# Kernel optimization log

Measured on AMD Instinct MI355X. Metric: run time of the kernel, lower is better.

The kernel has to match this reference:

```python
import jax, jax.numpy as jnp
import numpy as np

NUM_GRAPHS = 256
BN_EPS = 1e-5


def _bn(x, g, b, m, v):
    # eval-mode BatchNorm1d: affine with running stats
    return (x - m) * jax.lax.rsqrt(v + BN_EPS) * g + b


def setup_inputs() -> dict:
    key = jax.random.key(0)
    ks = jax.random.split(key, 16)
    N = 500_000
    x = jax.random.normal(ks[0], (N, 3), dtype=jnp.float32)
    batch = jnp.sort(jax.random.randint(ks[1], (N,), 0, NUM_GRAPHS, dtype=jnp.int32))

    def lin(k, fan_in, fan_out):
        kw, kb = jax.random.split(k)
        s = 1.0 / np.sqrt(fan_in)
        W = jax.random.uniform(kw, (fan_in, fan_out), jnp.float32, -s, s)
        b = jax.random.uniform(kb, (fan_out,), jnp.float32, -s, s)
        return W, b

    def bn_params(k, dim):
        k1, k2, k3, k4 = jax.random.split(k, 4)
        g = 1.0 + 0.05 * jax.random.normal(k1, (dim,), jnp.float32)
        be = 0.05 * jax.random.normal(k2, (dim,), jnp.float32)
        m = 0.05 * jax.random.normal(k3, (dim,), jnp.float32)
        v = 0.5 + jax.random.uniform(k4, (dim,), jnp.float32)
        return g, be, m, v

    W1, b1 = lin(ks[2], 3, 64)
    g1, be1, m1, v1 = bn_params(ks[3], 64)
    W2, b2 = lin(ks[4], 64, 64)          # plain last layer of local MLP
    W3, b3 = lin(ks[5], 64, 128)
    g3, be3, m3, v3 = bn_params(ks[6], 128)
    W4, b4 = lin(ks[7], 128, 1024)       # plain last layer of global MLP

    return {
        "x": x, "batch": batch,
        "W1": W1, "b1": b1, "g1": g1, "be1": be1, "m1": m1, "v1": v1,
        "W2": W2, "b2": b2,
        "W3": W3, "b3": b3, "g3": g3, "be3": be3, "m3": m3, "v3": v3,
        "W4": W4, "b4": b4,
    }


def reference(x, batch, W1, b1, g1, be1, m1, v1, W2, b2,
              W3, b3, g3, be3, m3, v3, W4, b4):
    # local MLP [3, 64, 64]: Linear->BN->ReLU, plain last
    h = jax.nn.relu(_bn(x @ W1 + b1, g1, be1, m1, v1))   # [N, 64]
    h = h @ W2 + b2                                       # [N, 64]
    # global MLP [64, 128, 1024]: Linear->BN->ReLU, plain last
    h = jax.nn.relu(_bn(h @ W3 + b3, g3, be3, m3, v3))    # [N, 128]
    h = h @ W4 + b4                                       # [N, 1024]
    # global_max_pool: ragged scatter-max over per-point graph ids
    out = jax.ops.segment_max(h, batch, num_segments=NUM_GRAPHS)  # [G, 1024]
    return out
```

## Files before the change

kernel.cpp:

```cpp
#include <hip/hip_runtime.h>
#include <hip/hip_bf16.h>
#include <cstdint>

typedef __attribute__((ext_vector_type(8))) short bf16x8;
typedef __attribute__((ext_vector_type(4))) float f32x4;

#define BN_EPS 1e-5f

__device__ __forceinline__ unsigned short f2bf(float f) {
    unsigned int u = __float_as_uint(f);
    unsigned int r = (u + 0x7FFFu + ((u >> 16) & 1u)) >> 16;
    return (unsigned short)r;
}
__device__ __forceinline__ float bf2f(unsigned short h) {
    return __uint_as_float(((unsigned int)h) << 16);
}
__device__ __forceinline__ unsigned int encf(float f) {
    unsigned int u = __float_as_uint(f);
    return (u & 0x80000000u) ? ~u : (u | 0x80000000u);
}

__device__ __forceinline__ long long lbound(const int* __restrict__ b, long long n, int key) {
    long long lo = 0, hi = n;
    while (lo < hi) { long long mid = (lo + hi) >> 1; if (b[mid] < key) lo = mid + 1; else hi = mid; }
    return lo;
}

__global__ void fold_kernel(const float* __restrict__ W1, const float* __restrict__ b1,
                            const float* __restrict__ g1, const float* __restrict__ be1,
                            const float* __restrict__ m1, const float* __restrict__ v1,
                            const float* __restrict__ W2, const float* __restrict__ b2,
                            const float* __restrict__ W3, const float* __restrict__ b3,
                            const float* __restrict__ g3, const float* __restrict__ be3,
                            const float* __restrict__ m3, const float* __restrict__ v3,
                            const float* __restrict__ W4,
                            unsigned short* __restrict__ W4p,
                            unsigned short* __restrict__ W23ph, unsigned short* __restrict__ W23pl,
                            float* __restrict__ W1c, float* __restrict__ b23) {
    int tid = blockIdx.x * blockDim.x + threadIdx.x;
    if (tid < 131072) {
        int j = tid & 7, lane = (tid >> 3) & 63, kf = (tid >> 9) & 3, nt = tid >> 11;
        int col = nt * 16 + (lane & 15);
        int k = kf * 32 + (lane >> 4) * 8 + j;
        W4p[tid] = f2bf(W4[k * 1024 + col]);
    }
    if (tid < 8192) {
        int j = tid & 7, lane = (tid >> 3) & 63, kf = (tid >> 9) & 1, nn = tid >> 10;
        int col = nn * 16 + (lane & 15);
        int k = kf * 32 + (lane >> 4) * 8 + j;
        float s3 = g3[col] / sqrtf(v3[col] + BN_EPS);
        float acc = 0.f;
        for (int o = 0; o < 64; ++o) acc += W2[k * 64 + o] * W3[o * 128 + col];
        float w = acc * s3;
        unsigned short hi = f2bf(w);
        W23ph[tid] = hi;
        W23pl[tid] = f2bf(w - bf2f(hi));
    }
    if (tid < 128) {
        float s3 = g3[tid] / sqrtf(v3[tid] + BN_EPS);
        float acc = b3[tid] - m3[tid];
        for (int o = 0; o < 64; ++o) acc += b2[o] * W3[o * 128 + tid];
        b23[tid] = acc * s3 + be3[tid];
    }
    if (tid < 256) {
        int o = tid >> 2, c = tid & 3;
        float s1 = g1[o] / sqrtf(v1[o] + BN_EPS);
        W1c[tid] = (c < 3) ? W1[c * 64 + o] * s1 : (b1[o] - m1[o]) * s1 + be1[o];
    }
}

__global__ __launch_bounds__(64, 4) void fused_kernel(const float* __restrict__ x,
                                                      const float* __restrict__ W1c,
                                                      const unsigned short* __restrict__ W23ph,
                                                      const unsigned short* __restrict__ W23pl,
                                                      const float* __restrict__ b23,
                                                      const unsigned short* __restrict__ W4p,
                                                      const float* __restrict__ b4,
                                                      const int* __restrict__ batch,
                                                      unsigned int* __restrict__ out,
                                                      float* __restrict__ tilemax,
                                                      int* __restrict__ gtile,
                                                      long long pbase, int ntiles, long long Ntot) {
    __shared__ unsigned short h3[64 * 72];
    int wave = blockIdx.x;
    if (wave >= ntiles) return;
    int lane = threadIdx.x & 63;
    int q = lane >> 4, r16 = lane & 15;
    long long p0 = pbase + (long long)wave * 64;

    float xv[4][3];
    bool valid[4];
#pragma unroll
    for (int mt = 0; mt < 4; ++mt) {
        long long p = p0 + mt * 16 + r16;
        if (p < Ntot) {
            xv[mt][0] = x[p * 3 + 0]; xv[mt][1] = x[p * 3 + 1]; xv[mt][2] = x[p * 3 + 2];
            valid[mt] = true;
        } else {
            xv[mt][0] = xv[mt][1] = xv[mt][2] = 0.f; valid[mt] = false;
        }
    }
    bf16x8 a2[4][2];
#pragma unroll
    for (int kf = 0; kf < 2; ++kf)
#pragma unroll
        for (int j = 0; j < 8; ++j) {
            int f = kf * 32 + q * 8 + j;
            float4 w = *reinterpret_cast<const float4*>(W1c + f * 4);
#pragma unroll
            for (int mt = 0; mt < 4; ++mt) {
                float v = fmaf(xv[mt][0], w.x, fmaf(xv[mt][1], w.y, fmaf(xv[mt][2], w.z, w.w)));
                v = valid[mt] ? fmaxf(v, 0.f) : 0.f;
                a2[mt][kf][j] = (short)f2bf(v);
            }
        }

    bf16x8 a[4][4];
#pragma unroll
    for (int half = 0; half < 2; ++half) {
#pragma unroll
        for (int n = 0; n < 4; ++n) {
            int nn = half * 4 + n;
            f32x4 acc2[4];
#pragma unroll
            for (int mt = 0; mt < 4; ++mt) acc2[mt] = (f32x4){0.f, 0.f, 0.f, 0.f};
#pragma unroll
            for (int kf = 0; kf < 2; ++kf) {
                bf16x8 bh = *reinterpret_cast<const bf16x8*>(W23ph + (size_t)((nn * 2 + kf) * 64 + lane) * 8);
                bf16x8 bl = *reinterpret_cast<const bf16x8*>(W23pl + (size_t)((nn * 2 + kf) * 64 + lane) * 8);
#pragma unroll
                for (int mt = 0; mt < 4; ++mt) {
                    acc2[mt] = __builtin_amdgcn_mfma_f32_16x16x32_bf16(a2[mt][kf], bh, acc2[mt], 0, 0, 0);
                    acc2[mt] = __builtin_amdgcn_mfma_f32_16x16x32_bf16(a2[mt][kf], bl, acc2[mt], 0, 0, 0);
                }
            }
            int col = nn * 16 + r16;
            float bias = b23[col];
#pragma unroll
            for (int mt = 0; mt < 4; ++mt)
#pragma unroll
                for (int r = 0; r < 4; ++r) {
                    int row = mt * 16 + q * 4 + r;
                    float v = fmaxf(acc2[mt][r] + bias, 0.f);
                    h3[row * 72 + n * 16 + r16] = f2bf(v);
                }
        }
        asm volatile("s_waitcnt lgkmcnt(0)" ::: "memory");
#pragma unroll
        for (int mt = 0; mt < 4; ++mt)
#pragma unroll
            for (int kfl = 0; kfl < 2; ++kfl)
                a[mt][half * 2 + kfl] =
                    *reinterpret_cast<const bf16x8*>(h3 + (16 * mt + r16) * 72 + kfl * 32 + q * 8);
        asm volatile("s_waitcnt lgkmcnt(0)" ::: "memory");
    }

    long long plast = p0 + 63; if (plast > Ntot - 1) plast = Ntot - 1;
    int gfirst = batch[(p0 < Ntot) ? p0 : (Ntot - 1)];
    int glast = batch[plast];
    bool fast = (gfirst == glast) && (p0 + 63 < Ntot);
    if (lane == 0) gtile[wave] = fast ? gfirst : -1;

    if (fast) {
        float* tm = tilemax + (size_t)wave * 1024;
        const unsigned short* wp = W4p + (size_t)lane * 8;
        bf16x8 Bp[2][4];
#pragma unroll
        for (int kf = 0; kf < 4; ++kf)
            Bp[0][kf] = *reinterpret_cast<const bf16x8*>(wp + (size_t)kf * 512);

        for (int g8 = 0; g8 < 8; ++g8) {
            float m8[8];
#pragma unroll
            for (int i8 = 0; i8 < 8; ++i8) {
                int nt = g8 * 8 + i8;
                const int cur = i8 & 1, nxt = cur ^ 1;
                {
                    const unsigned short* wq = wp + (size_t)(((nt + 1) & 63) * 4) * 512;
#pragma unroll
                    for (int kf = 0; kf < 4; ++kf)
                        Bp[nxt][kf] = *reinterpret_cast<const bf16x8*>(wq + (size_t)kf * 512);
                }
                f32x4 acc[4];
#pragma unroll
                for (int mt = 0; mt < 4; ++mt) acc[mt] = (f32x4){0.f, 0.f, 0.f, 0.f};
#pragma unroll
                for (int kf = 0; kf < 4; ++kf)
#pragma unroll
                    for (int mt = 0; mt < 4; ++mt)
                        acc[mt] = __builtin_amdgcn_mfma_f32_16x16x32_bf16(a[mt][kf], Bp[cur][kf], acc[mt], 0, 0, 0);
                float m = fmaxf(fmaxf(fmaxf(acc[0][0], acc[0][1]), fmaxf(acc[0][2], acc[0][3])),
                                fmaxf(fmaxf(acc[1][0], acc[1][1]), fmaxf(acc[1][2], acc[1][3])));
                m = fmaxf(m, fmaxf(fmaxf(fmaxf(acc[2][0], acc[2][1]), fmaxf(acc[2][2], acc[2][3])),
                                   fmaxf(fmaxf(acc[3][0], acc[3][1]), fmaxf(acc[3][2], acc[3][3]))));
                m8[i8] = m;
            }
#pragma unroll
            for (int qq = 0; qq < 8; ++qq) {
                float v = m8[qq];
                v = fmaxf(v, __shfl_xor(v, 16));
                v = fmaxf(v, __shfl_xor(v, 32));
                m8[qq] = v;
            }
            if (lane < 16) {
#pragma unroll
                for (int qq = 0; qq < 8; ++qq) tm[(g8 * 8 + qq) * 16 + lane] = m8[qq];
            }
        }
        return;
    }

    int gl = -1;
    unsigned long long smask = 0;
    int grow[16];
    {
        long long pl = p0 + lane;
        gl = (pl < Ntot) ? batch[pl] : -1;
        int gprev = __shfl_up(gl, 1);
        bool is_start = (lane == 0) || (gl != gprev);
        smask = __ballot(is_start);
#pragma unroll
        for (int m = 0; m < 4; ++m)
#pragma unroll
            for (int r = 0; r < 4; ++r) {
                int rw = m * 16 + (lane >> 4) * 4 + r;
                grow[m * 4 + r] = __shfl(gl, rw);
            }
    }

    for (int nt = 0; nt < 64; ++nt) {
        bf16x8 bq[4];
#pragma unroll
        for (int kf = 0; kf < 4; ++kf)
            bq[kf] = *reinterpret_cast<const bf16x8*>(W4p + (size_t)((nt * 4 + kf) * 64 + lane) * 8);
        f32x4 acc[4];
#pragma unroll
        for (int m = 0; m < 4; ++m) acc[m] = (f32x4){0.f, 0.f, 0.f, 0.f};
#pragma unroll
        for (int kf = 0; kf < 4; ++kf)
#pragma unroll
            for (int m = 0; m < 4; ++m)
                acc[m] = __builtin_amdgcn_mfma_f32_16x16x32_bf16(a[m][kf], bq[kf], acc[m], 0, 0, 0);

        int col = nt * 16 + (lane & 15);
        float bias = b4[col];
        unsigned long long tmp = smask;
        while (tmp) {
            int ls = __builtin_ctzll(tmp); tmp &= tmp - 1;
            int gs = __shfl(gl, ls);
            float m = -INFINITY;
#pragma unroll
            for (int mm = 0; mm < 4; ++mm)
#pragma unroll
                for (int r = 0; r < 4; ++r)
                    if (grow[mm * 4 + r] == gs) m = fmaxf(m, acc[mm][r]);
            m = fmaxf(m, __shfl_xor(m, 16));
            m = fmaxf(m, __shfl_xor(m, 32));
            if (gs >= 0 && lane < 16 && m > -INFINITY)
                atomicMax(&out[gs * 1024 + col], encf(m + bias));
        }
    }
}

__global__ __launch_bounds__(256) void reduce_chunk(const float* __restrict__ tilemax,
                                                    const int* __restrict__ gtile,
                                                    const int* __restrict__ batch,
                                                    const float* __restrict__ b4,
                                                    unsigned int* __restrict__ out,
                                                    long long base, long long npts, long long N) {
    int g = blockIdx.x >> 2;
    int col = (blockIdx.x & 3) * 256 + threadIdx.x;
    __shared__ int sh[2];
    if (threadIdx.x == 0) {
        long long lo = lbound(batch, N, g);
        long long hi = lbound(batch, N, g + 1);
        long long e = base + npts;
        if (lo < base) lo = base;
        if (hi > e) hi = e;
        sh[0] = (int)(lo - base);
        sh[1] = (int)(hi - base);
    }
    __syncthreads();
    int lo = sh[0], hi = sh[1];
    if (lo >= hi) return;
    int t0 = lo >> 6, t1 = (hi - 1) >> 6;
    float m = -INFINITY;
    for (int t = t0; t <= t1; ++t)
        if (gtile[t] == g) m = fmaxf(m, tilemax[(size_t)t * 1024 + col]);
    if (m > -INFINITY) atomicMax(&out[g * 1024 + col], encf(m + b4[col]));
}

__global__ void init_out(unsigned int* out, int n) {
    int t = blockIdx.x * 256 + threadIdx.x;
    if (t < n) out[t] = 0x007FFFFFu;
}
__global__ void decode_out(unsigned int* out, int n) {
    int t = blockIdx.x * 256 + threadIdx.x;
    if (t < n) {
        unsigned int e = out[t];
        out[t] = (e & 0x80000000u) ? (e & 0x7FFFFFFFu) : ~e;
    }
}

extern "C" void kernel_launch(void* const* d_in, const int* in_sizes, int n_in,
                              void* d_out, int out_size, void* d_ws, size_t ws_size,
                              hipStream_t stream) {
    const float* x   = (const float*)d_in[0];
    const int* batch = (const int*)d_in[1];
    const float* W1  = (const float*)d_in[2];
    const float* b1  = (const float*)d_in[3];
    const float* g1  = (const float*)d_in[4];
    const float* be1 = (const float*)d_in[5];
    const float* m1  = (const float*)d_in[6];
    const float* v1  = (const float*)d_in[7];
    const float* W2  = (const float*)d_in[8];
    const float* b2  = (const float*)d_in[9];
    const float* W3  = (const float*)d_in[10];
    const float* b3  = (const float*)d_in[11];
    const float* g3  = (const float*)d_in[12];
    const float* be3 = (const float*)d_in[13];
    const float* m3  = (const float*)d_in[14];
    const float* v3  = (const float*)d_in[15];
    const float* W4  = (const float*)d_in[16];
    const float* b4  = (const float*)d_in[17];

    long long N = in_sizes[1];

    char* ws = (char*)d_ws;
    unsigned short* W4p   = (unsigned short*)(ws + 0);
    unsigned short* W23ph = (unsigned short*)(ws + 262144);
    unsigned short* W23pl = (unsigned short*)(ws + 278528);
    float* W1c = (float*)(ws + 294912);
    float* b23 = (float*)(ws + 295936);

    fold_kernel<<<512, 256, 0, stream>>>(W1, b1, g1, be1, m1, v1, W2, b2, W3, b3, g3, be3, m3, v3,
                                         W4, W4p, W23ph, W23pl, W1c, b23);
    init_out<<<(out_size + 255) / 256, 256, 0, stream>>>((unsigned int*)d_out, out_size);

    const size_t ofs = 1 << 20;
    size_t avail = (ws_size > ofs) ? ws_size - ofs : 0;
    long long Tcap = (long long)(avail / 4104);
    Tcap &= ~3LL;
    if (Tcap < 4) Tcap = 4;
    long long ntiles_tot = (N + 63) / 64;
    long long ntcap = (ntiles_tot + 3) & ~3LL;
    if (Tcap > ntcap) Tcap = ntcap;

    float* tilemax = (float*)(ws + ofs);
    int* gtile = (int*)(ws + ofs + (size_t)Tcap * 4096);
    long long chunk = Tcap * 64;

    for (long long base = 0; base < N; base += chunk) {
        long long npts = N - base; if (npts > chunk) npts = chunk;
        int ntiles = (int)((npts + 63) / 64);
        fused_kernel<<<ntiles, 64, 0, stream>>>(x, W1c, W23ph, W23pl, b23, W4p, b4, batch,
                                                (unsigned int*)d_out, tilemax, gtile,
                                                base, ntiles, N);
        reduce_chunk<<<1024, 256, 0, stream>>>(tilemax, gtile, batch, b4, (unsigned int*)d_out,
                                               base, npts, N);
    }
    decode_out<<<(out_size + 255) / 256, 256, 0, stream>>>((unsigned int*)d_out, out_size);
}
```

Baseline: 207.6 us.

## Share W4 tiles across four waves via double-buffered LDS staging

The fused kernel now runs four 64-point tiles per 256-thread block. The W4 weights are streamed into a double-buffered LDS region with global_load_lds, and all four waves read them from there instead of each wave loading W4 from global/L2 on its own. The fast (single-graph) and slow (atomic) epilogues are merged into one loop, so every wave takes part in the block-wide barriers. This cuts global weight traffic, at the cost of a __syncthreads per group, more LDS per block (possibly lowering occupancy), and slow-path waves stalling the fast ones.

```diff
diff --git a/kernel.cpp b/kernel.cpp
--- a/kernel.cpp
+++ b/kernel.cpp
@@ -24,6 +24,12 @@
     long long lo = 0, hi = n;
     while (lo < hi) { long long mid = (lo + hi) >> 1; if (b[mid] < key) lo = mid + 1; else hi = mid; }
     return lo;
+}
+
+__device__ __forceinline__ void gl_lds16(const unsigned short* g, unsigned short* l) {
+    __builtin_amdgcn_global_load_lds((const __attribute__((address_space(1))) unsigned int*)g,
+                                     (__attribute__((address_space(3))) unsigned int*)l,
+                                     16, 0, 0);
 }
 
 __global__ void fold_kernel(const float* __restrict__ W1, const float* __restrict__ b1,
@@ -69,31 +75,33 @@
     }
 }
 
-__global__ __launch_bounds__(64, 4) void fused_kernel(const float* __restrict__ x,
-                                                      const float* __restrict__ W1c,
-                                                      const unsigned short* __restrict__ W23ph,
-                                                      const unsigned short* __restrict__ W23pl,
-                                                      const float* __restrict__ b23,
-                                                      const unsigned short* __restrict__ W4p,
-                                                      const float* __restrict__ b4,
-                                                      const int* __restrict__ batch,
-                                                      unsigned int* __restrict__ out,
-                                                      float* __restrict__ tilemax,
-                                                      int* __restrict__ gtile,
-                                                      long long pbase, int ntiles, long long Ntot) {
-    __shared__ unsigned short h3[64 * 72];
-    int wave = blockIdx.x;
-    if (wave >= ntiles) return;
+__global__ __launch_bounds__(256) void fused_kernel(const float* __restrict__ x,
+                                                    const float* __restrict__ W1c,
+                                                    const unsigned short* __restrict__ W23ph,
+                                                    const unsigned short* __restrict__ W23pl,
+                                                    const float* __restrict__ b23,
+                                                    const unsigned short* __restrict__ W4p,
+                                                    const float* __restrict__ b4,
+                                                    const int* __restrict__ batch,
+                                                    unsigned int* __restrict__ out,
+                                                    float* __restrict__ tilemax,
+                                                    int* __restrict__ gtile,
+                                                    long long pbase, int ntiles, long long Ntot) {
+    __shared__ unsigned short lds[18432];
+    int wv = threadIdx.x >> 6;
     int lane = threadIdx.x & 63;
+    int wave = blockIdx.x * 4 + wv;
+    bool active = wave < ntiles;
     int q = lane >> 4, r16 = lane & 15;
     long long p0 = pbase + (long long)wave * 64;
+    unsigned short* h3 = lds + wv * 4608;
 
     float xv[4][3];
     bool valid[4];
 #pragma unroll
     for (int mt = 0; mt < 4; ++mt) {
         long long p = p0 + mt * 16 + r16;
-        if (p < Ntot) {
+        if (active && p < Ntot) {
             xv[mt][0] = x[p * 3 + 0]; xv[mt][1] = x[p * 3 + 1]; xv[mt][2] = x[p * 3 + 2];
             valid[mt] = true;
         } else {
@@ -156,64 +164,16 @@
     }
 
     long long plast = p0 + 63; if (plast > Ntot - 1) plast = Ntot - 1;
-    int gfirst = batch[(p0 < Ntot) ? p0 : (Ntot - 1)];
+    long long pfirst = (p0 < Ntot) ? p0 : (Ntot - 1);
+    int gfirst = batch[pfirst];
     int glast = batch[plast];
-    bool fast = (gfirst == glast) && (p0 + 63 < Ntot);
-    if (lane == 0) gtile[wave] = fast ? gfirst : -1;
-
-    if (fast) {
-        float* tm = tilemax + (size_t)wave * 1024;
-        const unsigned short* wp = W4p + (size_t)lane * 8;
-        bf16x8 Bp[2][4];
-#pragma unroll
-        for (int kf = 0; kf < 4; ++kf)
-            Bp[0][kf] = *reinterpret_cast<const bf16x8*>(wp + (size_t)kf * 512);
-
-        for (int g8 = 0; g8 < 8; ++g8) {
-            float m8[8];
-#pragma unroll
-            for (int i8 = 0; i8 < 8; ++i8) {
-                int nt = g8 * 8 + i8;
-                const int cur = i8 & 1, nxt = cur ^ 1;
-                {
-                    const unsigned short* wq = wp + (size_t)(((nt + 1) & 63) * 4) * 512;
-#pragma unroll
-                    for (int kf = 0; kf < 4; ++kf)
-                        Bp[nxt][kf] = *reinterpret_cast<const bf16x8*>(wq + (size_t)kf * 512);
-                }
-                f32x4 acc[4];
-#pragma unroll
-                for (int mt = 0; mt < 4; ++mt) acc[mt] = (f32x4){0.f, 0.f, 0.f, 0.f};
-#pragma unroll
-                for (int kf = 0; kf < 4; ++kf)
-#pragma unroll
-                    for (int mt = 0; mt < 4; ++mt)
-                        acc[mt] = __builtin_amdgcn_mfma_f32_16x16x32_bf16(a[mt][kf], Bp[cur][kf], acc[mt], 0, 0, 0);
-                float m = fmaxf(fmaxf(fmaxf(acc[0][0], acc[0][1]), fmaxf(acc[0][2], acc[0][3])),
-                                fmaxf(fmaxf(acc[1][0], acc[1][1]), fmaxf(acc[1][2], acc[1][3])));
-                m = fmaxf(m, fmaxf(fmaxf(fmaxf(acc[2][0], acc[2][1]), fmaxf(acc[2][2], acc[2][3])),
-                                   fmaxf(fmaxf(acc[3][0], acc[3][1]), fmaxf(acc[3][2], acc[3][3]))));
-                m8[i8] = m;
-            }
-#pragma unroll
-            for (int qq = 0; qq < 8; ++qq) {
-                float v = m8[qq];
-                v = fmaxf(v, __shfl_xor(v, 16));
-                v = fmaxf(v, __shfl_xor(v, 32));
-                m8[qq] = v;
-            }
-            if (lane < 16) {
-#pragma unroll
-                for (int qq = 0; qq < 8; ++qq) tm[(g8 * 8 + qq) * 16 + lane] = m8[qq];
-            }
-        }
-        return;
-    }
+    bool fast = active && (gfirst == glast) && (p0 + 63 < Ntot);
+    if (active && lane == 0) gtile[wave] = fast ? gfirst : -1;
 
     int gl = -1;
     unsigned long long smask = 0;
     int grow[16];
-    {
+    if (active && !fast) {
         long long pl = p0 + lane;
         gl = (pl < Ntot) ? batch[pl] : -1;
         int gprev = __shfl_up(gl, 1);
@@ -228,37 +188,85 @@
             }
     }
 
-    for (int nt = 0; nt < 64; ++nt) {
-        bf16x8 bq[4];
-#pragma unroll
-        for (int kf = 0; kf < 4; ++kf)
-            bq[kf] = *reinterpret_cast<const bf16x8*>(W4p + (size_t)((nt * 4 + kf) * 64 + lane) * 8);
-        f32x4 acc[4];
-#pragma unroll
-        for (int m = 0; m < 4; ++m) acc[m] = (f32x4){0.f, 0.f, 0.f, 0.f};
-#pragma unroll
-        for (int kf = 0; kf < 4; ++kf)
-#pragma unroll
-            for (int m = 0; m < 4; ++m)
-                acc[m] = __builtin_amdgcn_mfma_f32_16x16x32_bf16(a[m][kf], bq[kf], acc[m], 0, 0, 0);
-
-        int col = nt * 16 + (lane & 15);
-        float bias = b4[col];
-        unsigned long long tmp = smask;
-        while (tmp) {
-            int ls = __builtin_ctzll(tmp); tmp &= tmp - 1;
-            int gs = __shfl(gl, ls);
-            float m = -INFINITY;
-#pragma unroll
-            for (int mm = 0; mm < 4; ++mm)
-#pragma unroll
-                for (int r = 0; r < 4; ++r)
-                    if (grow[mm * 4 + r] == gs) m = fmaxf(m, acc[mm][r]);
-            m = fmaxf(m, __shfl_xor(m, 16));
-            m = fmaxf(m, __shfl_xor(m, 32));
-            if (gs >= 0 && lane < 16 && m > -INFINITY)
-                atomicMax(&out[gs * 1024 + col], encf(m + bias));
-        }
+    float* tm = tilemax + (size_t)wave * 1024;
+
+    __syncthreads();
+    {
+        const unsigned short* src = W4p + wv * 2048 + lane * 8;
+        unsigned short* dst = lds + wv * 2048;
+#pragma unroll
+        for (int pass = 0; pass < 4; ++pass)
+            gl_lds16(src + pass * 512, dst + pass * 512);
+    }
+    __syncthreads();
+
+    for (int g = 0; g < 16; ++g) {
+        unsigned short* buf = lds + (g & 1) * 8192;
+        if (g < 15) {
+            const unsigned short* src = W4p + (size_t)(g + 1) * 8192 + wv * 2048 + lane * 8;
+            unsigned short* dst = lds + ((g + 1) & 1) * 8192 + wv * 2048;
+#pragma unroll
+            for (int pass = 0; pass < 4; ++pass)
+                gl_lds16(src + pass * 512, dst + pass * 512);
+        }
+
+        float m4[4];
+#pragma unroll
+        for (int l = 0; l < 4; ++l) {
+            bf16x8 bq[4];
+#pragma unroll
+            for (int kf = 0; kf < 4; ++kf)
+                bq[kf] = *reinterpret_cast<const bf16x8*>(buf + (l * 4 + kf) * 512 + lane * 8);
+            f32x4 acc[4];
+#pragma unroll
+            for (int mt = 0; mt < 4; ++mt) acc[mt] = (f32x4){0.f, 0.f, 0.f, 0.f};
+#pragma unroll
+            for (int kf = 0; kf < 4; ++kf)
+#pragma unroll
+                for (int mt = 0; mt < 4; ++mt)
+                    acc[mt] = __builtin_amdgcn_mfma_f32_16x16x32_bf16(a[mt][kf], bq[kf], acc[mt], 0, 0, 0);
+
+            if (fast) {
+                float m = fmaxf(fmaxf(fmaxf(acc[0][0], acc[0][1]), fmaxf(acc[0][2], acc[0][3])),
+                                fmaxf(fmaxf(acc[1][0], acc[1][1]), fmaxf(acc[1][2], acc[1][3])));
+                m = fmaxf(m, fmaxf(fmaxf(fmaxf(acc[2][0], acc[2][1]), fmaxf(acc[2][2], acc[2][3])),
+                                   fmaxf(fmaxf(acc[3][0], acc[3][1]), fmaxf(acc[3][2], acc[3][3]))));
+                m4[l] = m;
+            } else if (active) {
+                int nt = g * 4 + l;
+                int col = nt * 16 + (lane & 15);
+                float bias = b4[col];
+                unsigned long long tmp = smask;
+                while (tmp) {
+                    int ls = __builtin_ctzll(tmp); tmp &= tmp - 1;
+                    int gs = __shfl(gl, ls);
+                    float m = -INFINITY;
+#pragma unroll
+                    for (int mm = 0; mm < 4; ++mm)
+#pragma unroll
+                        for (int r = 0; r < 4; ++r)
+                            if (grow[mm * 4 + r] == gs) m = fmaxf(m, acc[mm][r]);
+                    m = fmaxf(m, __shfl_xor(m, 16));
+                    m = fmaxf(m, __shfl_xor(m, 32));
+                    if (gs >= 0 && lane < 16 && m > -INFINITY)
+                        atomicMax(&out[gs * 1024 + col], encf(m + bias));
+                }
+            }
+        }
+        if (fast) {
+#pragma unroll
+            for (int l = 0; l < 4; ++l) {
+                float v = m4[l];
+                v = fmaxf(v, __shfl_xor(v, 16));
+                v = fmaxf(v, __shfl_xor(v, 32));
+                m4[l] = v;
+            }
+            if (lane < 16) {
+#pragma unroll
+                for (int l = 0; l < 4; ++l) tm[(g * 4 + l) * 16 + lane] = m4[l];
+            }
+        }
+        __syncthreads();
     }
 }
 
@@ -353,9 +361,10 @@
     for (long long base = 0; base < N; base += chunk) {
         long long npts = N - base; if (npts > chunk) npts = chunk;
         int ntiles = (int)((npts + 63) / 64);
-        fused_kernel<<<ntiles, 64, 0, stream>>>(x, W1c, W23ph, W23pl, b23, W4p, b4, batch,
-                                                (unsigned int*)d_out, tilemax, gtile,
-                                                base, ntiles, N);
+        int blocks = (ntiles + 3) / 4;
+        fused_kernel<<<blocks, 256, 0, stream>>>(x, W1c, W23ph, W23pl, b23, W4p, b4, batch,
+                                                 (unsigned int*)d_out, tilemax, gtile,
+                                                 base, ntiles, N);
         reduce_chunk<<<1024, 256, 0, stream>>>(tilemax, gtile, batch, b4, (unsigned int*)d_out,
                                                base, npts, N);
     }
```

After: 224.7 us. 8.2% more time.

## Process two point tiles per wave sharing W4 fragment loads

Applied to the files above, without the earlier changes.

Each wave now computes the local MLP for two 64-point tiles and then runs the 1024-wide final GEMM for both at once. Every W4 fragment loaded from global memory feeds MFMAs for both tiles, which halves weight traffic per point and doubles independent MFMA chains per load. Blocks become two waves of 128 threads, and the LDS row stride is padded from 72 to 76. The cost is higher register pressure from two activation and accumulator sets, which may spill or cut occupancy, plus branchy mixing of fast and slow epilogues inside one loop.

```diff
diff --git a/kernel.cpp b/kernel.cpp
--- a/kernel.cpp
+++ b/kernel.cpp
@@ -69,31 +69,20 @@
     }
 }
 
-__global__ __launch_bounds__(64, 4) void fused_kernel(const float* __restrict__ x,
-                                                      const float* __restrict__ W1c,
-                                                      const unsigned short* __restrict__ W23ph,
-                                                      const unsigned short* __restrict__ W23pl,
-                                                      const float* __restrict__ b23,
-                                                      const unsigned short* __restrict__ W4p,
-                                                      const float* __restrict__ b4,
-                                                      const int* __restrict__ batch,
-                                                      unsigned int* __restrict__ out,
-                                                      float* __restrict__ tilemax,
-                                                      int* __restrict__ gtile,
-                                                      long long pbase, int ntiles, long long Ntot) {
-    __shared__ unsigned short h3[64 * 72];
-    int wave = blockIdx.x;
-    if (wave >= ntiles) return;
-    int lane = threadIdx.x & 63;
+__device__ __forceinline__ void mlp_tile(const float* __restrict__ x,
+                                         const float* __restrict__ W1c,
+                                         const unsigned short* __restrict__ W23ph,
+                                         const unsigned short* __restrict__ W23pl,
+                                         const float* __restrict__ b23,
+                                         unsigned short* h3, long long p0, bool act,
+                                         long long Ntot, int lane, bf16x8 (&a)[4][4]) {
     int q = lane >> 4, r16 = lane & 15;
-    long long p0 = pbase + (long long)wave * 64;
-
     float xv[4][3];
     bool valid[4];
 #pragma unroll
     for (int mt = 0; mt < 4; ++mt) {
         long long p = p0 + mt * 16 + r16;
-        if (p < Ntot) {
+        if (act && p < Ntot) {
             xv[mt][0] = x[p * 3 + 0]; xv[mt][1] = x[p * 3 + 1]; xv[mt][2] = x[p * 3 + 2];
             valid[mt] = true;
         } else {
@@ -114,8 +103,6 @@
                 a2[mt][kf][j] = (short)f2bf(v);
             }
         }
-
-    bf16x8 a[4][4];
 #pragma unroll
     for (int half = 0; half < 2; ++half) {
 #pragma unroll
@@ -142,7 +129,7 @@
                 for (int r = 0; r < 4; ++r) {
                     int row = mt * 16 + q * 4 + r;
                     float v = fmaxf(acc2[mt][r] + bias, 0.f);
-                    h3[row * 72 + n * 16 + r16] = f2bf(v);
+                    h3[row * 76 + n * 16 + r16] = f2bf(v);
                 }
         }
         asm volatile("s_waitcnt lgkmcnt(0)" ::: "memory");
@@ -151,113 +138,172 @@
 #pragma unroll
             for (int kfl = 0; kfl < 2; ++kfl)
                 a[mt][half * 2 + kfl] =
-                    *reinterpret_cast<const bf16x8*>(h3 + (16 * mt + r16) * 72 + kfl * 32 + q * 8);
+                    *reinterpret_cast<const bf16x8*>(h3 + (16 * mt + r16) * 76 + kfl * 32 + q * 8);
         asm volatile("s_waitcnt lgkmcnt(0)" ::: "memory");
     }
-
-    long long plast = p0 + 63; if (plast > Ntot - 1) plast = Ntot - 1;
-    int gfirst = batch[(p0 < Ntot) ? p0 : (Ntot - 1)];
-    int glast = batch[plast];
-    bool fast = (gfirst == glast) && (p0 + 63 < Ntot);
-    if (lane == 0) gtile[wave] = fast ? gfirst : -1;
-
-    if (fast) {
-        float* tm = tilemax + (size_t)wave * 1024;
-        const unsigned short* wp = W4p + (size_t)lane * 8;
-        bf16x8 Bp[2][4];
-#pragma unroll
-        for (int kf = 0; kf < 4; ++kf)
-            Bp[0][kf] = *reinterpret_cast<const bf16x8*>(wp + (size_t)kf * 512);
-
-        for (int g8 = 0; g8 < 8; ++g8) {
-            float m8[8];
-#pragma unroll
-            for (int i8 = 0; i8 < 8; ++i8) {
-                int nt = g8 * 8 + i8;
-                const int cur = i8 & 1, nxt = cur ^ 1;
-                {
-                    const unsigned short* wq = wp + (size_t)(((nt + 1) & 63) * 4) * 512;
-#pragma unroll
-                    for (int kf = 0; kf < 4; ++kf)
-                        Bp[nxt][kf] = *reinterpret_cast<const bf16x8*>(wq + (size_t)kf * 512);
+}
+
+__device__ __forceinline__ void slow_epi(const f32x4 (&acc)[4], int gl, unsigned long long smask,
+                                         int nt, int lane, const float* __restrict__ b4,
+                                         unsigned int* __restrict__ out) {
+    int col = nt * 16 + (lane & 15);
+    float bias = b4[col];
+    int grow[16];
+#pragma unroll
+    for (int m = 0; m < 4; ++m)
+#pragma unroll
+        for (int r = 0; r < 4; ++r)
+            grow[m * 4 + r] = __shfl(gl, m * 16 + (lane >> 4) * 4 + r);
+    unsigned long long tmp = smask;
+    while (tmp) {
+        int ls = __builtin_ctzll(tmp); tmp &= tmp - 1;
+        int gs = __shfl(gl, ls);
+        float m = -INFINITY;
+#pragma unroll
+        for (int mm = 0; mm < 4; ++mm)
+#pragma unroll
+            for (int r = 0; r < 4; ++r)
+                if (grow[mm * 4 + r] == gs) m = fmaxf(m, acc[mm][r]);
+        m = fmaxf(m, __shfl_xor(m, 16));
+        m = fmaxf(m, __shfl_xor(m, 32));
+        if (gs >= 0 && lane < 16 && m > -INFINITY)
+            atomicMax(&out[gs * 1024 + col], encf(m + bias));
+    }
+}
+
+__global__ __launch_bounds__(128, 2) void fused_kernel(const float* __restrict__ x,
+                                                       const float* __restrict__ W1c,
+                                                       const unsigned short* __restrict__ W23ph,
+                                                       const unsigned short* __restrict__ W23pl,
+                                                       const float* __restrict__ b23,
+                                                       const unsigned short* __restrict__ W4p,
+                                                       const float* __restrict__ b4,
+                                                       const int* __restrict__ batch,
+                                                       unsigned int* __restrict__ out,
+                                                       float* __restrict__ tilemax,
+                                                       int* __restrict__ gtile,
+                                                       long long pbase, int ntiles, long long Ntot) {
+    __shared__ unsigned short ldsbuf[2][64 * 76];
+    int wv = threadIdx.x >> 6;
+    int lane = threadIdx.x & 63;
+    int pair = blockIdx.x * 2 + wv;
+    int tile0 = pair * 2, tile1 = pair * 2 + 1;
+    if (tile0 >= ntiles) return;
+    bool active1 = tile1 < ntiles;
+    unsigned short* h3 = ldsbuf[wv];
+    long long p00 = pbase + (long long)tile0 * 64;
+    long long p01 = pbase + (long long)tile1 * 64;
+
+    bf16x8 a0[4][4], a1[4][4];
+    mlp_tile(x, W1c, W23ph, W23pl, b23, h3, p00, true, Ntot, lane, a0);
+    mlp_tile(x, W1c, W23ph, W23pl, b23, h3, p01, active1, Ntot, lane, a1);
+
+    long long pl0 = p00 + 63; if (pl0 > Ntot - 1) pl0 = Ntot - 1;
+    int gf0 = batch[p00];
+    bool fast0 = (gf0 == batch[pl0]) && (p00 + 63 < Ntot);
+    if (lane == 0) gtile[tile0] = fast0 ? gf0 : -1;
+    bool fast1 = false;
+    int gf1 = 0;
+    if (active1) {
+        long long pl1 = p01 + 63; if (pl1 > Ntot - 1) pl1 = Ntot - 1;
+        gf1 = batch[p01];
+        fast1 = (gf1 == batch[pl1]) && (p01 + 63 < Ntot);
+        if (lane == 0) gtile[tile1] = fast1 ? gf1 : -1;
+    }
+
+    int gl0 = -1, gl1 = -1;
+    unsigned long long smask0 = 0, smask1 = 0;
+    if (!fast0) {
+        long long pl = p00 + lane;
+        gl0 = (pl < Ntot) ? batch[pl] : -1;
+        int gprev = __shfl_up(gl0, 1);
+        smask0 = __ballot((lane == 0) || (gl0 != gprev));
+    }
+    if (active1 && !fast1) {
+        long long pl = p01 + lane;
+        gl1 = (pl < Ntot) ? batch[pl] : -1;
+        int gprev = __shfl_up(gl1, 1);
+        smask1 = __ballot((lane == 0) || (gl1 != gprev));
+    }
+
+    float* tm0 = tilemax + (size_t)tile0 * 1024;
+    float* tm1 = tilemax + (size_t)tile1 * 1024;
+    const unsigned short* wp = W4p + (size_t)lane * 8;
+
+    bf16x8 Bp[2][4];
+#pragma unroll
+    for (int kf = 0; kf < 4; ++kf)
+        Bp[0][kf] = *reinterpret_cast<const bf16x8*>(wp + (size_t)kf * 512);
+
+    for (int g4 = 0; g4 < 16; ++g4) {
+        float m40[4], m41[4];
+#pragma unroll
+        for (int i4 = 0; i4 < 4; ++i4) {
+            int nt = g4 * 4 + i4;
+            const int cur = nt & 1, nxt = cur ^ 1;
+            {
+                const unsigned short* wq = wp + (size_t)(((nt + 1) & 63) * 4) * 512;
+#pragma unroll
+                for (int kf = 0; kf < 4; ++kf)
+                    Bp[nxt][kf] = *reinterpret_cast<const bf16x8*>(wq + (size_t)kf * 512);
+            }
+            f32x4 acc0[4], acc1[4];
+#pragma unroll
+            for (int mt = 0; mt < 4; ++mt) {
+                acc0[mt] = (f32x4){0.f, 0.f, 0.f, 0.f};
+                acc1[mt] = (f32x4){0.f, 0.f, 0.f, 0.f};
+            }
+#pragma unroll
+            for (int kf = 0; kf < 4; ++kf)
+#pragma unroll
+                for (int mt = 0; mt < 4; ++mt) {
+                    acc0[mt] = __builtin_amdgcn_mfma_f32_16x16x32_bf16(a0[mt][kf], Bp[cur][kf], acc0[mt], 0, 0, 0);
+                    acc1[mt] = __builtin_amdgcn_mfma_f32_16x16x32_bf16(a1[mt][kf], Bp[cur][kf], acc1[mt], 0, 0, 0);
                 }
-                f32x4 acc[4];
-#pragma unroll
-                for (int mt = 0; mt < 4; ++mt) acc[mt] = (f32x4){0.f, 0.f, 0.f, 0.f};
-#pragma unroll
-                for (int kf = 0; kf < 4; ++kf)
-#pragma unroll
-                    for (int mt = 0; mt < 4; ++mt)
-                        acc[mt] = __builtin_amdgcn_mfma_f32_16x16x32_bf16(a[mt][kf], Bp[cur][kf], acc[mt], 0, 0, 0);
-                float m = fmaxf(fmaxf(fmaxf(acc[0][0], acc[0][1]), fmaxf(acc[0][2], acc[0][3])),
-                                fmaxf(fmaxf(acc[1][0], acc[1][1]), fmaxf(acc[1][2], acc[1][3])));
-                m = fmaxf(m, fmaxf(fmaxf(fmaxf(acc[2][0], acc[2][1]), fmaxf(acc[2][2], acc[2][3])),
-                                   fmaxf(fmaxf(acc[3][0], acc[3][1]), fmaxf(acc[3][2], acc[3][3]))));
-                m8[i8] = m;
-            }
-#pragma unroll
-            for (int qq = 0; qq < 8; ++qq) {
-                float v = m8[qq];
+            if (fast0) {
+                float m = fmaxf(fmaxf(fmaxf(acc0[0][0], acc0[0][1]), fmaxf(acc0[0][2], acc0[0][3])),
+                                fmaxf(fmaxf(acc0[1][0], acc0[1][1]), fmaxf(acc0[1][2], acc0[1][3])));
+                m = fmaxf(m, fmaxf(fmaxf(fmaxf(acc0[2][0], acc0[2][1]), fmaxf(acc0[2][2], acc0[2][3])),
+                                   fmaxf(fmaxf(acc0[3][0], acc0[3][1]), fmaxf(acc0[3][2], acc0[3][3]))));
+                m40[i4] = m;
+            } else {
+                slow_epi(acc0, gl0, smask0, nt, lane, b4, out);
+            }
+            if (fast1) {
+                float m = fmaxf(fmaxf(fmaxf(acc1[0][0], acc1[0][1]), fmaxf(acc1[0][2], acc1[0][3])),
+                                fmaxf(fmaxf(acc1[1][0], acc1[1][1]), fmaxf(acc1[1][2], acc1[1][3])));
+                m = fmaxf(m, fmaxf(fmaxf(fmaxf(acc1[2][0], acc1[2][1]), fmaxf(acc1[2][2], acc1[2][3])),
+                                   fmaxf(fmaxf(acc1[3][0], acc1[3][1]), fmaxf(acc1[3][2], acc1[3][3]))));
+                m41[i4] = m;
+            } else if (active1) {
+                slow_epi(acc1, gl1, smask1, nt, lane, b4, out);
+            }
+        }
+        if (fast0) {
+#pragma unroll
+            for (int l = 0; l < 4; ++l) {
+                float v = m40[l];
                 v = fmaxf(v, __shfl_xor(v, 16));
                 v = fmaxf(v, __shfl_xor(v, 32));
-                m8[qq] = v;
+                m40[l] = v;
             }
             if (lane < 16) {
 #pragma unroll
-                for (int qq = 0; qq < 8; ++qq) tm[(g8 * 8 + qq) * 16 + lane] = m8[qq];
-            }
-        }
-        return;
-    }
-
-    int gl = -1;
-    unsigned long long smask = 0;
-    int grow[16];
-    {
-        long long pl = p0 + lane;
-        gl = (pl < Ntot) ? batch[pl] : -1;
-        int gprev = __shfl_up(gl, 1);
-        bool is_start = (lane == 0) || (gl != gprev);
-        smask = __ballot(is_start);
-#pragma unroll
-        for (int m = 0; m < 4; ++m)
-#pragma unroll
-            for (int r = 0; r < 4; ++r) {
-                int rw = m * 16 + (lane >> 4) * 4 + r;
-                grow[m * 4 + r] = __shfl(gl, rw);
-            }
-    }
-
-    for (int nt = 0; nt < 64; ++nt) {
-        bf16x8 bq[4];
-#pragma unroll
-        for (int kf = 0; kf < 4; ++kf)
-            bq[kf] = *reinterpret_cast<const bf16x8*>(W4p + (size_t)((nt * 4 + kf) * 64 + lane) * 8);
-        f32x4 acc[4];
-#pragma unroll
-        for (int m = 0; m < 4; ++m) acc[m] = (f32x4){0.f, 0.f, 0.f, 0.f};
-#pragma unroll
-        for (int kf = 0; kf < 4; ++kf)
-#pragma unroll
-            for (int m = 0; m < 4; ++m)
-                acc[m] = __builtin_amdgcn_mfma_f32_16x16x32_bf16(a[m][kf], bq[kf], acc[m], 0, 0, 0);
-
-        int col = nt * 16 + (lane & 15);
-        float bias = b4[col];
-        unsigned long long tmp = smask;
-        while (tmp) {
-            int ls = __builtin_ctzll(tmp); tmp &= tmp - 1;
-            int gs = __shfl(gl, ls);
-            float m = -INFINITY;
-#pragma unroll
-            for (int mm = 0; mm < 4; ++mm)
-#pragma unroll
-                for (int r = 0; r < 4; ++r)
-                    if (grow[mm * 4 + r] == gs) m = fmaxf(m, acc[mm][r]);
-            m = fmaxf(m, __shfl_xor(m, 16));
-            m = fmaxf(m, __shfl_xor(m, 32));
-            if (gs >= 0 && lane < 16 && m > -INFINITY)
-                atomicMax(&out[gs * 1024 + col], encf(m + bias));
+                for (int l = 0; l < 4; ++l) tm0[(g4 * 4 + l) * 16 + lane] = m40[l];
+            }
+        }
+        if (fast1) {
+#pragma unroll
+            for (int l = 0; l < 4; ++l) {
+                float v = m41[l];
+                v = fmaxf(v, __shfl_xor(v, 16));
+                v = fmaxf(v, __shfl_xor(v, 32));
+                m41[l] = v;
+            }
+            if (lane < 16) {
+#pragma unroll
+                for (int l = 0; l < 4; ++l) tm1[(g4 * 4 + l) * 16 + lane] = m41[l];
+            }
         }
     }
 }
@@ -353,9 +399,11 @@
     for (long long base = 0; base < N; base += chunk) {
         long long npts = N - base; if (npts > chunk) npts = chunk;
         int ntiles = (int)((npts + 63) / 64);
-        fused_kernel<<<ntiles, 64, 0, stream>>>(x, W1c, W23ph, W23pl, b23, W4p, b4, batch,
-                                                (unsigned int*)d_out, tilemax, gtile,
-                                                base, ntiles, N);
+        int npairs = (ntiles + 1) / 2;
+        int blocks = (npairs + 1) / 2;
+        fused_kernel<<<blocks, 128, 0, stream>>>(x, W1c, W23ph, W23pl, b23, W4p, b4, batch,
+                                                 (unsigned int*)d_out, tilemax, gtile,
+                                                 base, ntiles, N);
         reduce_chunk<<<1024, 256, 0, stream>>>(tilemax, gtile, batch, b4, (unsigned int*)d_out,
                                                base, npts, N);
     }
```

Measured after the change: 228.4 us. +10.0%, slower.
